# Performance work log

Hardware: AMD Instinct MI355X
Metric: run time of the kernel (lower is better)

Reference implementation:

```python
import jax, jax.numpy as jnp
import numpy as np

B = 32768
F = 256
H = 8


def setup_inputs() -> dict:
    key = jax.random.key(0)
    ks = jax.random.split(key, 6)
    input_tensor = jax.random.normal(ks[0], (B, F), dtype=jnp.float32)
    # Per-feature MLP params: Dense(1->8), Dense(8->8), Dense(8->1, no bias)
    W1 = jax.random.normal(ks[1], (F, H), dtype=jnp.float32) * 0.5   # [F, 8] (input dim 1 folded)
    b1 = jax.random.normal(ks[2], (F, H), dtype=jnp.float32) * 0.1
    W2 = jax.random.normal(ks[3], (F, H, H), dtype=jnp.float32) * (1.0 / np.sqrt(H))
    b2 = jax.random.normal(ks[4], (F, H), dtype=jnp.float32) * 0.1
    W3 = jax.random.normal(ks[5], (F, H), dtype=jnp.float32) * (1.0 / np.sqrt(H))  # [F, 8] (output dim 1 folded)
    return {"input_tensor": input_tensor, "W1": W1, "b1": b1, "W2": W2, "b2": b2, "W3": W3}


def reference(input_tensor, W1, b1, W2, b2, W3):
    # Batched over features instead of a Python loop over F tiny MLPs.
    # h1: [B, F, H] = relu(x * W1 + b1), scalar input per feature
    h1 = jax.nn.relu(input_tensor[:, :, None] * W1[None, :, :] + b1[None, :, :])
    # h2: [B, F, H]
    h2 = jax.nn.relu(jnp.einsum('bfh,fhk->bfk', h1, W2) + b2[None, :, :])
    # per-feature scalar contribution w: [B, F]
    w = jnp.einsum('bfh,fh->bf', h2, W3)
    output = jnp.sum(w, axis=1, keepdims=True)  # [B, 1]
    return (output, w)
```

## Files before the change

### kernel.cpp

```cpp
#include <hip/hip_runtime.h>

#define NB 32768
#define NF 256
#define NH 8
#define ROWS_PER_BLOCK 8

__global__ __launch_bounds__(256, 3) void NAM_49314814493074_kernel(
    const float* __restrict__ input,
    const float* __restrict__ W1,
    const float* __restrict__ b1,
    const float* __restrict__ W2,
    const float* __restrict__ b2,
    const float* __restrict__ W3,
    float* __restrict__ out_sum,
    float* __restrict__ out_w)
{
    __shared__ float sred[ROWS_PER_BLOCK][NF];

    const int f = threadIdx.x;
    const int row0 = blockIdx.x * ROWS_PER_BLOCK;

    const float* xin = input + (size_t)row0 * NF + f;

    float xv[ROWS_PER_BLOCK];
    #pragma unroll
    for (int r = 0; r < ROWS_PER_BLOCK; ++r)
        xv[r] = xin[(size_t)r * NF];

    float w1[NH], bb1[NH], bb2[NH], w3[NH];
    float w2[NH][NH];
    {
        const float4* p1  = reinterpret_cast<const float4*>(W1 + (size_t)f * NH);
        const float4* pb1 = reinterpret_cast<const float4*>(b1 + (size_t)f * NH);
        const float4* pb2 = reinterpret_cast<const float4*>(b2 + (size_t)f * NH);
        const float4* p3  = reinterpret_cast<const float4*>(W3 + (size_t)f * NH);
        float4 a, b;
        a = p1[0]; b = p1[1];
        w1[0]=a.x; w1[1]=a.y; w1[2]=a.z; w1[3]=a.w; w1[4]=b.x; w1[5]=b.y; w1[6]=b.z; w1[7]=b.w;
        a = pb1[0]; b = pb1[1];
        bb1[0]=a.x; bb1[1]=a.y; bb1[2]=a.z; bb1[3]=a.w; bb1[4]=b.x; bb1[5]=b.y; bb1[6]=b.z; bb1[7]=b.w;
        a = pb2[0]; b = pb2[1];
        bb2[0]=a.x; bb2[1]=a.y; bb2[2]=a.z; bb2[3]=a.w; bb2[4]=b.x; bb2[5]=b.y; bb2[6]=b.z; bb2[7]=b.w;
        a = p3[0]; b = p3[1];
        w3[0]=a.x; w3[1]=a.y; w3[2]=a.z; w3[3]=a.w; w3[4]=b.x; w3[5]=b.y; w3[6]=b.z; w3[7]=b.w;

        const float4* p2 = reinterpret_cast<const float4*>(W2 + (size_t)f * NH * NH);
        #pragma unroll
        for (int h = 0; h < NH; ++h) {
            float4 c0 = p2[h * 2 + 0];
            float4 c1 = p2[h * 2 + 1];
            w2[h][0]=c0.x; w2[h][1]=c0.y; w2[h][2]=c0.z; w2[h][3]=c0.w;
            w2[h][4]=c1.x; w2[h][5]=c1.y; w2[h][6]=c1.z; w2[h][7]=c1.w;
        }
    }

    #pragma unroll
    for (int r = 0; r < ROWS_PER_BLOCK; ++r) {
        const float x = xv[r];

        float h1[NH];
        #pragma unroll
        for (int h = 0; h < NH; ++h)
            h1[h] = fmaxf(fmaf(x, w1[h], bb1[h]), 0.0f);

        float acc[NH];
        #pragma unroll
        for (int k = 0; k < NH; ++k)
            acc[k] = fmaf(h1[0], w2[0][k], bb2[k]);
        #pragma unroll
        for (int h = 1; h < NH; ++h) {
            #pragma unroll
            for (int k = 0; k < NH; ++k)
                acc[k] = fmaf(h1[h], w2[h][k], acc[k]);
        }

        float s = 0.0f;
        #pragma unroll
        for (int k = 0; k < NH; ++k)
            s = fmaf(fmaxf(acc[k], 0.0f), w3[k], s);

        sred[r][f] = s;
    }

    __syncthreads();

    const int wave = threadIdx.x >> 6;
    const int lane = threadIdx.x & 63;
    #pragma unroll
    for (int rr = 0; rr < ROWS_PER_BLOCK / 4; ++rr) {
        const int r = wave * (ROWS_PER_BLOCK / 4) + rr;
        const float4 q = reinterpret_cast<const float4*>(&sred[r][0])[lane];
        reinterpret_cast<float4*>(out_w + (size_t)(row0 + r) * NF)[lane] = q;
        float v = q.x + q.y + q.z + q.w;
        #pragma unroll
        for (int off = 32; off > 0; off >>= 1)
            v += __shfl_xor(v, off, 64);
        if (lane == 0)
            out_sum[row0 + r] = v;
    }
}

extern "C" void kernel_launch(void* const* d_in, const int* in_sizes, int n_in,
                              void* d_out, int out_size, void* d_ws, size_t ws_size,
                              hipStream_t stream) {
    const float* input = (const float*)d_in[0];
    const float* W1    = (const float*)d_in[1];
    const float* b1    = (const float*)d_in[2];
    const float* W2    = (const float*)d_in[3];
    const float* b2    = (const float*)d_in[4];
    const float* W3    = (const float*)d_in[5];

    float* out = (float*)d_out;
    float* out_sum = out;
    float* out_w   = out + NB;

    dim3 grid(NB / ROWS_PER_BLOCK);
    dim3 block(NF);
    NAM_49314814493074_kernel<<<grid, block, 0, stream>>>(
        input, W1, b1, W2, b2, W3, out_sum, out_w);
}
```

Baseline: 122.6 us.

## Stage input rows into LDS via direct global_load_lds and process 32 rows per block

Input rows are now loaded straight into shared memory with the global_load_lds builtin and issued before the per-feature weights are read, so the two loads can overlap. Each block now handles 32 rows instead of 8, so the 88 weight floats per feature are loaded once per 32 rows, and the results reuse the same LDS buffer. Weights are kept in vector registers, and empty asm barriers force them to load early. The costs are a 4x smaller grid (1024 blocks, which may leave CUs underfilled) and 32KB of LDS per block, which limits occupancy.

```diff
diff --git a/kernel.cpp b/kernel.cpp
--- a/kernel.cpp
+++ b/kernel.cpp
@@ -3,7 +3,12 @@
 #define NB 32768
 #define NF 256
 #define NH 8
-#define ROWS_PER_BLOCK 8
+#define RPB 32
+
+
+typedef float f4 __attribute__((ext_vector_type(4)));
+typedef __attribute__((address_space(1))) const unsigned int gu32;
+typedef __attribute__((address_space(3))) unsigned int lu32;
 
 __global__ __launch_bounds__(256, 3) void NAM_49314814493074_kernel(
     const float* __restrict__ input,
@@ -15,81 +20,82 @@
     float* __restrict__ out_sum,
     float* __restrict__ out_w)
 {
-    __shared__ float sred[ROWS_PER_BLOCK][NF];
+    __shared__ float xs[RPB][NF];
 
-    const int f = threadIdx.x;
-    const int row0 = blockIdx.x * ROWS_PER_BLOCK;
+    const int f    = threadIdx.x;
+    const int wave = f >> 6;
+    const int lane = f & 63;
+    const int row0 = blockIdx.x * RPB;
 
-    const float* xin = input + (size_t)row0 * NF + f;
-
-    float xv[ROWS_PER_BLOCK];
-    #pragma unroll
-    for (int r = 0; r < ROWS_PER_BLOCK; ++r)
-        xv[r] = xin[(size_t)r * NF];
-
-    float w1[NH], bb1[NH], bb2[NH], w3[NH];
-    float w2[NH][NH];
     {
-        const float4* p1  = reinterpret_cast<const float4*>(W1 + (size_t)f * NH);
-        const float4* pb1 = reinterpret_cast<const float4*>(b1 + (size_t)f * NH);
-        const float4* pb2 = reinterpret_cast<const float4*>(b2 + (size_t)f * NH);
-        const float4* p3  = reinterpret_cast<const float4*>(W3 + (size_t)f * NH);
-        float4 a, b;
-        a = p1[0]; b = p1[1];
-        w1[0]=a.x; w1[1]=a.y; w1[2]=a.z; w1[3]=a.w; w1[4]=b.x; w1[5]=b.y; w1[6]=b.z; w1[7]=b.w;
-        a = pb1[0]; b = pb1[1];
-        bb1[0]=a.x; bb1[1]=a.y; bb1[2]=a.z; bb1[3]=a.w; bb1[4]=b.x; bb1[5]=b.y; bb1[6]=b.z; bb1[7]=b.w;
-        a = pb2[0]; b = pb2[1];
-        bb2[0]=a.x; bb2[1]=a.y; bb2[2]=a.z; bb2[3]=a.w; bb2[4]=b.x; bb2[5]=b.y; bb2[6]=b.z; bb2[7]=b.w;
-        a = p3[0]; b = p3[1];
-        w3[0]=a.x; w3[1]=a.y; w3[2]=a.z; w3[3]=a.w; w3[4]=b.x; w3[5]=b.y; w3[6]=b.z; w3[7]=b.w;
-
-        const float4* p2 = reinterpret_cast<const float4*>(W2 + (size_t)f * NH * NH);
+        const float* g = input + (size_t)row0 * NF + wave * 64 + lane;
+        float* l = &xs[0][wave * 64];
         #pragma unroll
-        for (int h = 0; h < NH; ++h) {
-            float4 c0 = p2[h * 2 + 0];
-            float4 c1 = p2[h * 2 + 1];
-            w2[h][0]=c0.x; w2[h][1]=c0.y; w2[h][2]=c0.z; w2[h][3]=c0.w;
-            w2[h][4]=c1.x; w2[h][5]=c1.y; w2[h][6]=c1.z; w2[h][7]=c1.w;
+        for (int r = 0; r < RPB; ++r) {
+            __builtin_amdgcn_global_load_lds((gu32*)(g + (size_t)r * NF),
+                                             (lu32*)(l + r * NF), 4, 0, 0);
         }
     }
 
+    f4 w1a, w1b, b1a, b1b, b2a, b2b, w3a, w3b, w2v[16];
+    {
+        const f4* pW1 = reinterpret_cast<const f4*>(W1 + (size_t)f * NH);
+        const f4* pB1 = reinterpret_cast<const f4*>(b1 + (size_t)f * NH);
+        const f4* pB2 = reinterpret_cast<const f4*>(b2 + (size_t)f * NH);
+        const f4* pW3 = reinterpret_cast<const f4*>(W3 + (size_t)f * NH);
+        const f4* pW2 = reinterpret_cast<const f4*>(W2 + (size_t)f * NH * NH);
+        w1a = pW1[0]; w1b = pW1[1];
+        b1a = pB1[0]; b1b = pB1[1];
+        b2a = pB2[0]; b2b = pB2[1];
+        w3a = pW3[0]; w3b = pW3[1];
+        #pragma unroll
+        for (int i = 0; i < 16; ++i) w2v[i] = pW2[i];
+    }
+    asm volatile("" : "+v"(w1a), "+v"(w1b), "+v"(b1a), "+v"(b1b),
+                      "+v"(b2a), "+v"(b2b), "+v"(w3a), "+v"(w3b));
+    asm volatile("" : "+v"(w2v[0]), "+v"(w2v[1]), "+v"(w2v[2]), "+v"(w2v[3]),
+                      "+v"(w2v[4]), "+v"(w2v[5]), "+v"(w2v[6]), "+v"(w2v[7]),
+                      "+v"(w2v[8]), "+v"(w2v[9]), "+v"(w2v[10]), "+v"(w2v[11]),
+                      "+v"(w2v[12]), "+v"(w2v[13]), "+v"(w2v[14]), "+v"(w2v[15]));
+
+    __syncthreads();
+
     #pragma unroll
-    for (int r = 0; r < ROWS_PER_BLOCK; ++r) {
-        const float x = xv[r];
+    for (int r = 0; r < RPB; ++r) {
+        const float x = xs[r][f];
 
         float h1[NH];
         #pragma unroll
         for (int h = 0; h < NH; ++h)
-            h1[h] = fmaxf(fmaf(x, w1[h], bb1[h]), 0.0f);
+            h1[h] = fmaxf(fmaf(x, (h < 4 ? w1a[h] : w1b[h - 4]),
+                                  (h < 4 ? b1a[h] : b1b[h - 4])), 0.0f);
 
         float acc[NH];
         #pragma unroll
         for (int k = 0; k < NH; ++k)
-            acc[k] = fmaf(h1[0], w2[0][k], bb2[k]);
+            acc[k] = fmaf(h1[0], w2v[(k >> 2)][k & 3],
+                          (k < 4 ? b2a[k] : b2b[k - 4]));
         #pragma unroll
         for (int h = 1; h < NH; ++h) {
             #pragma unroll
             for (int k = 0; k < NH; ++k)
-                acc[k] = fmaf(h1[h], w2[h][k], acc[k]);
+                acc[k] = fmaf(h1[h], w2v[h * 2 + (k >> 2)][k & 3], acc[k]);
         }
 
         float s = 0.0f;
         #pragma unroll
         for (int k = 0; k < NH; ++k)
-            s = fmaf(fmaxf(acc[k], 0.0f), w3[k], s);
+            s = fmaf(fmaxf(acc[k], 0.0f), (k < 4 ? w3a[k] : w3b[k - 4]), s);
 
-        sred[r][f] = s;
+        xs[r][f] = s;
     }
 
     __syncthreads();
 
-    const int wave = threadIdx.x >> 6;
-    const int lane = threadIdx.x & 63;
     #pragma unroll
-    for (int rr = 0; rr < ROWS_PER_BLOCK / 4; ++rr) {
-        const int r = wave * (ROWS_PER_BLOCK / 4) + rr;
-        const float4 q = reinterpret_cast<const float4*>(&sred[r][0])[lane];
+    for (int rr = 0; rr < RPB / 4; ++rr) {
+        const int r = wave * (RPB / 4) + rr;
+        const float4 q = reinterpret_cast<const float4*>(&xs[r][0])[lane];
         reinterpret_cast<float4*>(out_w + (size_t)(row0 + r) * NF)[lane] = q;
         float v = q.x + q.y + q.z + q.w;
         #pragma unroll
@@ -114,7 +120,7 @@
     float* out_sum = out;
     float* out_w   = out + NB;
 
-    dim3 grid(NB / ROWS_PER_BLOCK);
+    dim3 grid(NB / RPB);
     dim3 block(NF);
     NAM_49314814493074_kernel<<<grid, block, 0, stream>>>(
         input, W1, b1, W2, b2, W3, out_sum, out_w);
```

Measured after the change: 109.7 us. -10.5%, faster.
